# Kernel tuning notes

Measured on AMD Instinct MI355X. Metric: run time of the kernel, lower is better.

Reference implementation:

```python
import math
import jax, jax.numpy as jnp
import numpy as np

B, T = 64, 8192
D_OUT = 128
KPOS = 2
DT = 1.0 / 240.0


def _ema(x, alpha):
    # x: [B, T] -> causal EMA along T: acc = alpha*acc + (1-alpha)*x_t, acc0 = 0
    def step(acc, xt):
        acc = alpha * acc + (1.0 - alpha) * xt
        return acc, acc
    _, ys = jax.lax.scan(step, jnp.zeros(x.shape[0], x.dtype), x.T)  # ys: [T, B]
    return ys.T


def _fourier_axis(coord, logw, phi):
    # coord: [B,T]; logw, phi: [K] -> [B,T,2K]
    w = jnp.exp(logw)[None, None, :]
    arg = 2.0 * math.pi * coord[..., None] * w + phi[None, None, :]
    return jnp.concatenate([jnp.sin(arg), jnp.cos(arg)], axis=-1)


def setup_inputs() -> dict:
    key = jax.random.key(0)
    ks = jax.random.split(key, 4)
    gaze_xy = jax.random.normal(ks[0], (B, T, 2), dtype=jnp.float32) * 5.0
    D_in = 4 * KPOS + 12  # 20
    # xavier-uniform style init for the two Linear layers
    lim1 = math.sqrt(6.0 / (D_in + D_OUT))
    lim2 = math.sqrt(6.0 / (D_OUT + D_OUT))
    W1 = jax.random.uniform(ks[1], (D_in, D_OUT), jnp.float32, -lim1, lim1)
    b1 = jnp.zeros((D_OUT,), jnp.float32)
    W2 = jax.random.uniform(ks[2], (D_OUT, D_OUT), jnp.float32, -lim2, lim2)
    b2 = jnp.zeros((D_OUT,), jnp.float32)
    return {
        "gaze_xy": gaze_xy,
        "pos_logw_x": jnp.full((KPOS,), math.log(1.0 / 64.0), jnp.float32),
        "pos_phi_x": jnp.zeros((KPOS,), jnp.float32),
        "pos_logw_y": jnp.full((KPOS,), math.log(1.0 / 64.0), jnp.float32),
        "pos_phi_y": jnp.zeros((KPOS,), jnp.float32),
        "sac_log_thr": jnp.asarray(math.log(200.0), jnp.float32),
        "sac_invT": jnp.asarray(0.05, jnp.float32),
        "W1": W1, "b1": b1, "W2": W2, "b2": b2,
    }


def reference(gaze_xy, pos_logw_x, pos_phi_x, pos_logw_y, pos_phi_y,
              sac_log_thr, sac_invT, W1, b1, W2, b2):
    dt = max(DT, 1e-6)
    eps = 1e-6
    # causal diff with first-frame prepend (diff at t=0 is zero)
    prev = jnp.concatenate([gaze_xy[:, :1], gaze_xy[:, :-1]], axis=1)
    v = (gaze_xy - prev) / dt                      # [B,T,2]
    v_prev = jnp.concatenate([v[:, :1], v[:, :-1]], axis=1)
    a = (v - v_prev) / dt                          # [B,T,2]
    speed = jnp.linalg.norm(v, axis=-1)            # [B,T]
    inv_sp = 1.0 / (speed + eps)
    dir_cos = v[..., 0] * inv_sp
    dir_sin = v[..., 1] * inv_sp
    a_par = (v * a).sum(-1) * inv_sp
    a_perp = (v[..., 0] * a[..., 1] - v[..., 1] * a[..., 0]) * inv_sp
    thr = jnp.exp(sac_log_thr)
    gate = jax.nn.sigmoid(sac_invT * (speed - thr))  # [B,T]
    q_fast = _ema(gate, 0.8)
    q_slow = _ema(gate, 0.95)
    scalars = jnp.stack([v[..., 0], v[..., 1], speed, dir_cos, dir_sin,
                         a[..., 0], a[..., 1], a_par, a_perp,
                         gate, q_fast, q_slow], axis=-1)  # [B,T,12]
    fx = _fourier_axis(gaze_xy[..., 0], pos_logw_x, pos_phi_x)  # [B,T,4]
    fy = _fourier_axis(gaze_xy[..., 1], pos_logw_y, pos_phi_y)  # [B,T,4]
    feats = jnp.concatenate([fx, fy, scalars], axis=-1)         # [B,T,20]
    h = jax.nn.gelu(feats @ W1 + b1, approximate=False)
    h = jax.nn.gelu(h @ W2 + b2, approximate=False)
    return h
```

## Files before the change

### kernel.cpp

```cpp
#include <hip/hip_runtime.h>
#include <math.h>

#define BB 64
#define TT 8192
#define NTILES 8192
#define MLP_GRID 768
#define EMA_GRID 512

typedef short short8 __attribute__((ext_vector_type(8)));
typedef float f32x4 __attribute__((ext_vector_type(4)));

__device__ __forceinline__ unsigned short f2bf(float x) {
    unsigned int u = __float_as_uint(x);
    u += 0x7fffu + ((u >> 16) & 1u);
    return (unsigned short)(u >> 16);
}

__device__ __forceinline__ unsigned int f2bf2(float lo, float hi) {
    return (unsigned int)f2bf(lo) | ((unsigned int)f2bf(hi) << 16);
}

__device__ __forceinline__ float fast_sigmoid(float z) {
    return __builtin_amdgcn_rcpf(1.0f + __expf(-z));
}

__device__ __forceinline__ float fast_gelu(float x) {
    return x * fast_sigmoid(1.702f * x);
}

__global__ __launch_bounds__(256) void ema_kernel(
    const float* __restrict__ gaze, const float* __restrict__ logthr,
    const float* __restrict__ invT, float* __restrict__ qf, float* __restrict__ qs)
{
    __shared__ __align__(16) float sg[1280];
    const int tid = threadIdx.x;
    const int b   = blockIdx.x >> 3;
    const int t0  = (blockIdx.x & 7) << 10;
    const float thr = __expf(logthr[0]);
    const float sT  = invT[0];
    const float2* gz = (const float2*)gaze + (size_t)b * TT;

    #pragma unroll
    for (int it = 0; it < 5; ++it) {
        int i = tid + it * 256;
        int t = t0 - 252 + i;
        float val = 0.0f;
        if (t >= 0 && t < TT) {
            float vx = 0.0f, vy = 0.0f;
            if (t > 0) {
                float2 a = gz[t], p = gz[t - 1];
                vx = (a.x - p.x) * 240.0f;
                vy = (a.y - p.y) * 240.0f;
            }
            float speed = sqrtf(vx * vx + vy * vy);
            val = 1.0f / (1.0f + __expf(-sT * (speed - thr)));
        }
        sg[i] = val;
    }
    __syncthreads();

    const float4* sg4 = (const float4*)sg;
    float Sf = 0.0f, Ss = 0.0f;
    float wf = 0.16f;
    float ws = 0.0475f;
    for (int u = 62; u >= 0; --u) {
        float4 qv = sg4[tid + u];
        float hf = fmaf(0.8f,  fmaf(0.8f,  fmaf(0.8f,  qv.x, qv.y), qv.z), qv.w);
        Sf = fmaf(wf, hf, Sf);  wf *= 0.4096f;
        float hs = fmaf(0.95f, fmaf(0.95f, fmaf(0.95f, qv.x, qv.y), qv.z), qv.w);
        Ss = fmaf(ws, hs, Ss);  ws *= 0.81450625f;
    }
    float4 r = sg4[tid + 63];
    float g0v = r.x, g1v = r.y, g2v = r.z, g3v = r.w;

    float o0 = Sf + 0.2f * g0v;
    float o1 = fmaf(0.8f,   Sf, 0.2f * fmaf(0.8f, g0v, g1v));
    float o2 = fmaf(0.64f,  Sf, 0.2f * (g2v + 0.8f * g1v + 0.64f * g0v));
    float o3 = fmaf(0.512f, Sf, 0.2f * (g3v + 0.8f * g2v + 0.64f * g1v + 0.512f * g0v));

    float p0 = Ss + 0.05f * g0v;
    float p1 = fmaf(0.95f,     Ss, 0.05f * fmaf(0.95f, g0v, g1v));
    float p2 = fmaf(0.9025f,   Ss, 0.05f * (g2v + 0.95f * g1v + 0.9025f * g0v));
    float p3 = fmaf(0.857375f, Ss, 0.05f * (g3v + 0.95f * g2v + 0.9025f * g1v + 0.857375f * g0v));

    const size_t ob = (size_t)b * TT + t0 + 4 * tid;
    *(float4*)(qf + ob) = make_float4(o0, o1, o2, o3);
    *(float4*)(qs + ob) = make_float4(p0, p1, p2, p3);
}

__global__ __launch_bounds__(256, 3) void mlp_kernel(
    const float* __restrict__ gaze,
    const float* __restrict__ lwx, const float* __restrict__ phx,
    const float* __restrict__ lwy, const float* __restrict__ phy,
    const float* __restrict__ logthr, const float* __restrict__ invT,
    const float* __restrict__ W1, const float* __restrict__ b1,
    const float* __restrict__ W2, const float* __restrict__ b2,
    const float* __restrict__ qf, const float* __restrict__ qs,
    float* __restrict__ out)
{
    __shared__ __align__(16) unsigned short sW2[128 * 136];
    __shared__ __align__(16) unsigned short sh1[4][16 * 136];

    const int tid  = threadIdx.x;
    const int wave = tid >> 6;
    const int lane = tid & 63;
    const int c    = lane & 15;
    const int q    = lane >> 4;

    #pragma unroll
    for (int it = 0; it < 32; ++it) {
        int i  = tid + it * 256;
        int n  = i & 127;
        int kp = i >> 7;
        unsigned short lo = f2bf(W2[(2 * kp) * 128 + n]);
        unsigned short hi = f2bf(W2[(2 * kp + 1) * 128 + n]);
        *(unsigned int*)&sW2[n * 136 + 2 * kp] = ((unsigned int)hi << 16) | lo;
    }

    short8 B1[8];
    #pragma unroll
    for (int j = 0; j < 8; ++j) {
        union { unsigned short u[8]; short8 v; } tmp;
        #pragma unroll
        for (int u = 0; u < 8; ++u) {
            int k = 8 * q + u;
            float w = 0.0f;
            if (k < 20)       w = W1[k * 128 + 16 * j + c];
            else if (k == 20) w = b1[16 * j + c];
            tmp.u[u] = (k <= 20) ? f2bf(w) : (unsigned short)0;
        }
        B1[j] = tmp.v;
    }

    f32x4 bias2v[8];
    #pragma unroll
    for (int j = 0; j < 8; ++j)
        bias2v[j] = *(const f32x4*)&b2[16 * j + 4 * q];

    const float twopi = 6.283185307179586f;
    const float cwx0 = twopi * __expf(lwx[0]), cwx1 = twopi * __expf(lwx[1]);
    const float cwy0 = twopi * __expf(lwy[0]), cwy1 = twopi * __expf(lwy[1]);
    const float px0 = phx[0], px1 = phx[1], py0 = phy[0], py1 = phy[1];
    const float thr = __expf(logthr[0]), sT = invT[0];

    __syncthreads();

    unsigned short* h1w = sh1[wave];
    const float2* gz = (const float2*)gaze;

    for (int tile = blockIdx.x; tile < NTILES; tile += MLP_GRID) {
        const int b   = tile >> 7;
        const int t0  = (tile & 127) << 6;
        const int t   = t0 + wave * 16 + c;
        const int idx = b * TT + t;

        float2 g0 = gz[idx];
        float2 g1 = (t > 0) ? gz[idx - 1] : g0;
        float2 g2 = (t > 1) ? gz[idx - 2] : g1;
        float vx = (g0.x - g1.x) * 240.0f;
        float vy = (g0.y - g1.y) * 240.0f;
        float vpx = (g1.x - g2.x) * 240.0f;
        float vpy = (g1.y - g2.y) * 240.0f;
        float ax = (vx - vpx) * 240.0f;
        float ay = (vy - vpy) * 240.0f;
        float speed  = sqrtf(vx * vx + vy * vy);
        float inv_sp = __builtin_amdgcn_rcpf(speed + 1e-6f);

        float f[8] = {0.f, 0.f, 0.f, 0.f, 0.f, 0.f, 0.f, 0.f};
        if (q == 0) {
            __sincosf(fmaf(g0.x, cwx0, px0), &f[0], &f[2]);
            __sincosf(fmaf(g0.x, cwx1, px1), &f[1], &f[3]);
            __sincosf(fmaf(g0.y, cwy0, py0), &f[4], &f[6]);
            __sincosf(fmaf(g0.y, cwy1, py1), &f[5], &f[7]);
        } else if (q == 1) {
            f[0] = vx; f[1] = vy; f[2] = speed;
            f[3] = vx * inv_sp; f[4] = vy * inv_sp;
            f[5] = ax; f[6] = ay;
            f[7] = (vx * ax + vy * ay) * inv_sp;
        } else if (q == 2) {
            f[0] = (vx * ay - vy * ax) * inv_sp;
            f[1] = fast_sigmoid(sT * (speed - thr));
            f[2] = qf[idx];
            f[3] = qs[idx];
            f[4] = 1.0f;
        }

        union { unsigned short u[8]; short8 v; } A1;
        #pragma unroll
        for (int k = 0; k < 8; ++k) A1.u[k] = f2bf(f[k]);

        #pragma unroll
        for (int j = 0; j < 8; ++j) {
            f32x4 acc = {0.f, 0.f, 0.f, 0.f};
            acc = __builtin_amdgcn_mfma_f32_16x16x32_bf16(B1[j], A1.v, acc, 0, 0, 0);
            unsigned int lo = f2bf2(fast_gelu(acc[0]), fast_gelu(acc[1]));
            unsigned int hi = f2bf2(fast_gelu(acc[2]), fast_gelu(acc[3]));
            *(uint2*)&h1w[c * 136 + 16 * j + 4 * q] = make_uint2(lo, hi);
        }
        asm volatile("s_waitcnt lgkmcnt(0)" ::: "memory");

        short8 A2[4];
        #pragma unroll
        for (int s = 0; s < 4; ++s)
            A2[s] = *(const short8*)&h1w[c * 136 + 32 * s + 8 * q];

        float* ob = out + (size_t)(b * TT + t0 + wave * 16 + c) * 128 + 4 * q;
        #pragma unroll
        for (int j = 0; j < 8; ++j) {
            f32x4 acc = bias2v[j];
            #pragma unroll
            for (int s = 0; s < 4; ++s) {
                short8 W2f = *(const short8*)&sW2[(16 * j + c) * 136 + 32 * s + 8 * q];
                acc = __builtin_amdgcn_mfma_f32_16x16x32_bf16(W2f, A2[s], acc, 0, 0, 0);
            }
            f32x4 o;
            #pragma unroll
            for (int r = 0; r < 4; ++r) o[r] = fast_gelu(acc[r]);
            __builtin_nontemporal_store(o, (f32x4*)(ob + 16 * j));
        }
    }
}

extern "C" void kernel_launch(void* const* d_in, const int* in_sizes, int n_in,
                              void* d_out, int out_size, void* d_ws, size_t ws_size,
                              hipStream_t stream)
{
    const float* gaze   = (const float*)d_in[0];
    const float* lwx    = (const float*)d_in[1];
    const float* phx    = (const float*)d_in[2];
    const float* lwy    = (const float*)d_in[3];
    const float* phy    = (const float*)d_in[4];
    const float* logthr = (const float*)d_in[5];
    const float* invT   = (const float*)d_in[6];
    const float* W1     = (const float*)d_in[7];
    const float* b1     = (const float*)d_in[8];
    const float* W2     = (const float*)d_in[9];
    const float* b2     = (const float*)d_in[10];
    float* out = (float*)d_out;

    float* qf = (float*)d_ws;
    float* qs = qf + BB * TT;

    ema_kernel<<<EMA_GRID, 256, 0, stream>>>(gaze, logthr, invT, qf, qs);
    mlp_kernel<<<MLP_GRID, 256, 0, stream>>>(gaze, lwx, phx, lwy, phy, logthr, invT,
                                             W1, b1, W2, b2, qf, qs, out);
}
```

Before: 327.2 us.

## Use 512-thread MLP blocks with software-prefetched inputs and LDS bias

The MLP kernel now runs 8 waves per block, each covering 128 time steps per tile, on a grid of 512 blocks. The gaze and EMA inputs for the next tile are loaded into registers while the current tile is computed, so global load latency is hidden. The b2 bias moves from registers to shared memory to cut register pressure for the higher occupancy target. This costs extra registers for the prefetched values and a per-tile LDS read of the bias.

New measurement: 339.1 us. +3.6%, slower.

```diff
diff --git a/kernel.cpp b/kernel.cpp
--- a/kernel.cpp
+++ b/kernel.cpp
@@ -3,8 +3,8 @@
 
 #define BB 64
 #define TT 8192
-#define NTILES 8192
-#define MLP_GRID 768
+#define NT2 4096
+#define MLP_GRID 512
 #define EMA_GRID 512
 
 typedef short short8 __attribute__((ext_vector_type(8)));
@@ -88,7 +88,7 @@
     *(float4*)(qs + ob) = make_float4(p0, p1, p2, p3);
 }
 
-__global__ __launch_bounds__(256, 3) void mlp_kernel(
+__global__ __launch_bounds__(512, 4) void mlp_kernel(
     const float* __restrict__ gaze,
     const float* __restrict__ lwx, const float* __restrict__ phx,
     const float* __restrict__ lwy, const float* __restrict__ phy,
@@ -99,7 +99,8 @@
     float* __restrict__ out)
 {
     __shared__ __align__(16) unsigned short sW2[128 * 136];
-    __shared__ __align__(16) unsigned short sh1[4][16 * 136];
+    __shared__ __align__(16) unsigned short sh1[8][16 * 136];
+    __shared__ __align__(16) float sb2[128];
 
     const int tid  = threadIdx.x;
     const int wave = tid >> 6;
@@ -108,14 +109,15 @@
     const int q    = lane >> 4;
 
     #pragma unroll
-    for (int it = 0; it < 32; ++it) {
-        int i  = tid + it * 256;
+    for (int it = 0; it < 16; ++it) {
+        int i  = tid + it * 512;
         int n  = i & 127;
         int kp = i >> 7;
         unsigned short lo = f2bf(W2[(2 * kp) * 128 + n]);
         unsigned short hi = f2bf(W2[(2 * kp + 1) * 128 + n]);
         *(unsigned int*)&sW2[n * 136 + 2 * kp] = ((unsigned int)hi << 16) | lo;
     }
+    if (tid < 128) sb2[tid] = b2[tid];
 
     short8 B1[8];
     #pragma unroll
@@ -132,11 +134,6 @@
         B1[j] = tmp.v;
     }
 
-    f32x4 bias2v[8];
-    #pragma unroll
-    for (int j = 0; j < 8; ++j)
-        bias2v[j] = *(const f32x4*)&b2[16 * j + 4 * q];
-
     const float twopi = 6.283185307179586f;
     const float cwx0 = twopi * __expf(lwx[0]), cwx1 = twopi * __expf(lwx[1]);
     const float cwy0 = twopi * __expf(lwy[0]), cwy1 = twopi * __expf(lwy[1]);
@@ -148,15 +145,35 @@
     unsigned short* h1w = sh1[wave];
     const float2* gz = (const float2*)gaze;
 
-    for (int tile = blockIdx.x; tile < NTILES; tile += MLP_GRID) {
-        const int b   = tile >> 7;
-        const int t0  = (tile & 127) << 6;
+    int tile = blockIdx.x;
+    float2 g0, g1, g2; float qfv = 0.f, qsv = 0.f;
+    {
+        const int b   = tile >> 6;
+        const int t   = ((tile & 63) << 7) + wave * 16 + c;
+        const int idx = b * TT + t;
+        g0 = gz[idx];
+        g1 = (t > 0) ? gz[idx - 1] : g0;
+        g2 = (t > 1) ? gz[idx - 2] : g1;
+        if (q == 2) { qfv = qf[idx]; qsv = qs[idx]; }
+    }
+
+    for (; tile < NT2; tile += MLP_GRID) {
+        const int b   = tile >> 6;
+        const int t0  = (tile & 63) << 7;
         const int t   = t0 + wave * 16 + c;
-        const int idx = b * TT + t;
-
-        float2 g0 = gz[idx];
-        float2 g1 = (t > 0) ? gz[idx - 1] : g0;
-        float2 g2 = (t > 1) ? gz[idx - 2] : g1;
+
+        float2 n0 = g0, n1 = g1, n2 = g2; float nqf = 0.f, nqs = 0.f;
+        const int ntile = tile + MLP_GRID;
+        if (ntile < NT2) {
+            const int nb   = ntile >> 6;
+            const int nt   = ((ntile & 63) << 7) + wave * 16 + c;
+            const int nidx = nb * TT + nt;
+            n0 = gz[nidx];
+            n1 = (nt > 0) ? gz[nidx - 1] : n0;
+            n2 = (nt > 1) ? gz[nidx - 2] : n1;
+            if (q == 2) { nqf = qf[nidx]; nqs = qs[nidx]; }
+        }
+
         float vx = (g0.x - g1.x) * 240.0f;
         float vy = (g0.y - g1.y) * 240.0f;
         float vpx = (g1.x - g2.x) * 240.0f;
@@ -180,8 +197,8 @@
         } else if (q == 2) {
             f[0] = (vx * ay - vy * ax) * inv_sp;
             f[1] = fast_sigmoid(sT * (speed - thr));
-            f[2] = qf[idx];
-            f[3] = qs[idx];
+            f[2] = qfv;
+            f[3] = qsv;
             f[4] = 1.0f;
         }
 
@@ -207,7 +224,7 @@
         float* ob = out + (size_t)(b * TT + t0 + wave * 16 + c) * 128 + 4 * q;
         #pragma unroll
         for (int j = 0; j < 8; ++j) {
-            f32x4 acc = bias2v[j];
+            f32x4 acc = *(const f32x4*)&sb2[16 * j + 4 * q];
             #pragma unroll
             for (int s = 0; s < 4; ++s) {
                 short8 W2f = *(const short8*)&sW2[(16 * j + c) * 136 + 32 * s + 8 * q];
@@ -218,6 +235,8 @@
             for (int r = 0; r < 4; ++r) o[r] = fast_gelu(acc[r]);
             __builtin_nontemporal_store(o, (f32x4*)(ob + 16 * j));
         }
+
+        g0 = n0; g1 = n1; g2 = n2; qfv = nqf; qsv = nqs;
     }
 }
 
@@ -242,6 +261,6 @@
     float* qs = qf + BB * TT;
 
     ema_kernel<<<EMA_GRID, 256, 0, stream>>>(gaze, logthr, invT, qf, qs);
-    mlp_kernel<<<MLP_GRID, 256, 0, stream>>>(gaze, lwx, phx, lwy, phy, logthr, invT,
+    mlp_kernel<<<MLP_GRID, 512, 0, stream>>>(gaze, lwx, phx, lwy, phy, logthr, invT,
                                              W1, b1, W2, b2, qf, qs, out);
 }
```

## Pre-convert weights to bf16 in prep kernel and read them from global/L1

Applied to the files above, without the earlier changes.

Adds a small prep kernel that converts W1 (plus bias row) and W2 to bf16 in the workspace once per call. The MLP kernel drops its per-block LDS staging of W2 and its register-held W1 fragments, and instead loads weight fragments from global memory inside the tile loop, relying on cache. It also raises occupancy (launch bounds 4, grid 1024). This removes per-block conversion work and frees LDS and registers, at the cost of repeated global/L1 weight loads per tile and an extra kernel launch.

New measurement: 398.5 us. 1.22x slower.

```diff
diff --git a/kernel.cpp b/kernel.cpp
--- a/kernel.cpp
+++ b/kernel.cpp
@@ -4,7 +4,7 @@
 #define BB 64
 #define TT 8192
 #define NTILES 8192
-#define MLP_GRID 768
+#define MLP_GRID 1024
 #define EMA_GRID 512
 
 typedef short short8 __attribute__((ext_vector_type(8)));
@@ -26,6 +26,25 @@
 
 __device__ __forceinline__ float fast_gelu(float x) {
     return x * fast_sigmoid(1.702f * x);
+}
+
+__global__ __launch_bounds__(256) void prep_kernel(
+    const float* __restrict__ W1, const float* __restrict__ b1,
+    const float* __restrict__ W2,
+    unsigned short* __restrict__ w1bf, unsigned short* __restrict__ w2bf)
+{
+    const int tid = threadIdx.x;
+    const int bid = blockIdx.x;
+    if (bid < 64) {
+        int i  = bid * 256 + tid;
+        int ch = i >> 7, k = i & 127;
+        w2bf[i] = f2bf(W2[k * 128 + ch]);
+    } else {
+        int i  = (bid - 64) * 256 + tid;
+        int ch = i >> 5, k = i & 31;
+        float v = (k < 20) ? W1[k * 128 + ch] : ((k == 20) ? b1[ch] : 0.0f);
+        w1bf[i] = f2bf(v);
+    }
 }
 
 __global__ __launch_bounds__(256) void ema_kernel(
@@ -88,17 +107,16 @@
     *(float4*)(qs + ob) = make_float4(p0, p1, p2, p3);
 }
 
-__global__ __launch_bounds__(256, 3) void mlp_kernel(
+__global__ __launch_bounds__(256, 4) void mlp_kernel(
     const float* __restrict__ gaze,
     const float* __restrict__ lwx, const float* __restrict__ phx,
     const float* __restrict__ lwy, const float* __restrict__ phy,
     const float* __restrict__ logthr, const float* __restrict__ invT,
-    const float* __restrict__ W1, const float* __restrict__ b1,
-    const float* __restrict__ W2, const float* __restrict__ b2,
+    const unsigned short* __restrict__ w1bf, const unsigned short* __restrict__ w2bf,
+    const float* __restrict__ b2,
     const float* __restrict__ qf, const float* __restrict__ qs,
     float* __restrict__ out)
 {
-    __shared__ __align__(16) unsigned short sW2[128 * 136];
     __shared__ __align__(16) unsigned short sh1[4][16 * 136];
 
     const int tid  = threadIdx.x;
@@ -107,44 +125,12 @@
     const int c    = lane & 15;
     const int q    = lane >> 4;
 
-    #pragma unroll
-    for (int it = 0; it < 32; ++it) {
-        int i  = tid + it * 256;
-        int n  = i & 127;
-        int kp = i >> 7;
-        unsigned short lo = f2bf(W2[(2 * kp) * 128 + n]);
-        unsigned short hi = f2bf(W2[(2 * kp + 1) * 128 + n]);
-        *(unsigned int*)&sW2[n * 136 + 2 * kp] = ((unsigned int)hi << 16) | lo;
-    }
-
-    short8 B1[8];
-    #pragma unroll
-    for (int j = 0; j < 8; ++j) {
-        union { unsigned short u[8]; short8 v; } tmp;
-        #pragma unroll
-        for (int u = 0; u < 8; ++u) {
-            int k = 8 * q + u;
-            float w = 0.0f;
-            if (k < 20)       w = W1[k * 128 + 16 * j + c];
-            else if (k == 20) w = b1[16 * j + c];
-            tmp.u[u] = (k <= 20) ? f2bf(w) : (unsigned short)0;
-        }
-        B1[j] = tmp.v;
-    }
-
-    f32x4 bias2v[8];
-    #pragma unroll
-    for (int j = 0; j < 8; ++j)
-        bias2v[j] = *(const f32x4*)&b2[16 * j + 4 * q];
-
     const float twopi = 6.283185307179586f;
     const float cwx0 = twopi * __expf(lwx[0]), cwx1 = twopi * __expf(lwx[1]);
     const float cwy0 = twopi * __expf(lwy[0]), cwy1 = twopi * __expf(lwy[1]);
     const float px0 = phx[0], px1 = phx[1], py0 = phy[0], py1 = phy[1];
     const float thr = __expf(logthr[0]), sT = invT[0];
 
-    __syncthreads();
-
     unsigned short* h1w = sh1[wave];
     const float2* gz = (const float2*)gaze;
 
@@ -153,6 +139,14 @@
         const int t0  = (tile & 127) << 6;
         const int t   = t0 + wave * 16 + c;
         const int idx = b * TT + t;
+
+        unsigned long long a1 = (unsigned long long)w1bf;
+        unsigned long long a2 = (unsigned long long)w2bf;
+        unsigned long long a3 = (unsigned long long)b2;
+        asm volatile("" : "+s"(a1), "+s"(a2), "+s"(a3));
+        const unsigned short* w1p = (const unsigned short*)a1;
+        const unsigned short* w2p = (const unsigned short*)a2;
+        const float*          b2p = (const float*)a3;
 
         float2 g0 = gz[idx];
         float2 g1 = (t > 0) ? gz[idx - 1] : g0;
@@ -191,8 +185,9 @@
 
         #pragma unroll
         for (int j = 0; j < 8; ++j) {
+            short8 B1j = *(const short8*)&w1p[(16 * j + c) * 32 + 8 * q];
             f32x4 acc = {0.f, 0.f, 0.f, 0.f};
-            acc = __builtin_amdgcn_mfma_f32_16x16x32_bf16(B1[j], A1.v, acc, 0, 0, 0);
+            acc = __builtin_amdgcn_mfma_f32_16x16x32_bf16(B1j, A1.v, acc, 0, 0, 0);
             unsigned int lo = f2bf2(fast_gelu(acc[0]), fast_gelu(acc[1]));
             unsigned int hi = f2bf2(fast_gelu(acc[2]), fast_gelu(acc[3]));
             *(uint2*)&h1w[c * 136 + 16 * j + 4 * q] = make_uint2(lo, hi);
@@ -207,10 +202,10 @@
         float* ob = out + (size_t)(b * TT + t0 + wave * 16 + c) * 128 + 4 * q;
         #pragma unroll
         for (int j = 0; j < 8; ++j) {
-            f32x4 acc = bias2v[j];
+            f32x4 acc = *(const f32x4*)&b2p[16 * j + 4 * q];
             #pragma unroll
             for (int s = 0; s < 4; ++s) {
-                short8 W2f = *(const short8*)&sW2[(16 * j + c) * 136 + 32 * s + 8 * q];
+                short8 W2f = *(const short8*)&w2p[(16 * j + c) * 128 + 32 * s + 8 * q];
                 acc = __builtin_amdgcn_mfma_f32_16x16x32_bf16(W2f, A2[s], acc, 0, 0, 0);
             }
             f32x4 o;
@@ -240,8 +235,11 @@
 
     float* qf = (float*)d_ws;
     float* qs = qf + BB * TT;
-
+    unsigned short* w1bf = (unsigned short*)(qs + BB * TT);
+    unsigned short* w2bf = w1bf + 128 * 32;
+
+    prep_kernel<<<80, 256, 0, stream>>>(W1, b1, W2, w1bf, w2bf);
     ema_kernel<<<EMA_GRID, 256, 0, stream>>>(gaze, logthr, invT, qf, qs);
     mlp_kernel<<<MLP_GRID, 256, 0, stream>>>(gaze, lwx, phx, lwy, phy, logthr, invT,
-                                             W1, b1, W2, b2, qf, qs, out);
-}
+                                             w1bf, w2bf, b2, qf, qs, out);
+}
```

## Permute W1 columns so layer-1 MFMA output feeds layer-2 directly in registers

Applied to the files above, without the earlier changes.

Reorders the hidden-channel mapping of W1/b1 so each lane's layer-1 accumulator values line up with the bf16 A-operand layout needed by the layer-2 MFMA. This removes the per-wave shared-memory round trip and its wait for the hidden activations. The b2 bias moves from registers to LDS, and the grid grows with launch bounds raised to 4 blocks per SIMD to increase occupancy, which tightens the register budget and could cause spills.

Result: no change. 326.6 us (-0.2%).

```diff
diff --git a/kernel.cpp b/kernel.cpp
--- a/kernel.cpp
+++ b/kernel.cpp
@@ -4,7 +4,7 @@
 #define BB 64
 #define TT 8192
 #define NTILES 8192
-#define MLP_GRID 768
+#define MLP_GRID 2048
 #define EMA_GRID 512
 
 typedef short short8 __attribute__((ext_vector_type(8)));
@@ -88,7 +88,7 @@
     *(float4*)(qs + ob) = make_float4(p0, p1, p2, p3);
 }
 
-__global__ __launch_bounds__(256, 3) void mlp_kernel(
+__global__ __launch_bounds__(256, 4) void mlp_kernel(
     const float* __restrict__ gaze,
     const float* __restrict__ lwx, const float* __restrict__ phx,
     const float* __restrict__ lwy, const float* __restrict__ phy,
@@ -99,11 +99,11 @@
     float* __restrict__ out)
 {
     __shared__ __align__(16) unsigned short sW2[128 * 136];
-    __shared__ __align__(16) unsigned short sh1[4][16 * 136];
+    __shared__ __align__(16) float sb2[128];
 
     const int tid  = threadIdx.x;
+    const int lane = tid & 63;
     const int wave = tid >> 6;
-    const int lane = tid & 63;
     const int c    = lane & 15;
     const int q    = lane >> 4;
 
@@ -116,26 +116,23 @@
         unsigned short hi = f2bf(W2[(2 * kp + 1) * 128 + n]);
         *(unsigned int*)&sW2[n * 136 + 2 * kp] = ((unsigned int)hi << 16) | lo;
     }
+    if (tid < 128) sb2[tid] = b2[tid];
 
     short8 B1[8];
     #pragma unroll
     for (int j = 0; j < 8; ++j) {
+        const int ch = 32 * (j & 3) + 8 * (c >> 2) + 4 * (j >> 2) + (c & 3);
         union { unsigned short u[8]; short8 v; } tmp;
         #pragma unroll
         for (int u = 0; u < 8; ++u) {
             int k = 8 * q + u;
             float w = 0.0f;
-            if (k < 20)       w = W1[k * 128 + 16 * j + c];
-            else if (k == 20) w = b1[16 * j + c];
+            if (k < 20)       w = W1[k * 128 + ch];
+            else if (k == 20) w = b1[ch];
             tmp.u[u] = (k <= 20) ? f2bf(w) : (unsigned short)0;
         }
         B1[j] = tmp.v;
     }
-
-    f32x4 bias2v[8];
-    #pragma unroll
-    for (int j = 0; j < 8; ++j)
-        bias2v[j] = *(const f32x4*)&b2[16 * j + 4 * q];
 
     const float twopi = 6.283185307179586f;
     const float cwx0 = twopi * __expf(lwx[0]), cwx1 = twopi * __expf(lwx[1]);
@@ -145,7 +142,6 @@
 
     __syncthreads();
 
-    unsigned short* h1w = sh1[wave];
     const float2* gz = (const float2*)gaze;
 
     for (int tile = blockIdx.x; tile < NTILES; tile += MLP_GRID) {
@@ -189,25 +185,28 @@
         #pragma unroll
         for (int k = 0; k < 8; ++k) A1.u[k] = f2bf(f[k]);
 
+        f32x4 acc1[8];
         #pragma unroll
         for (int j = 0; j < 8; ++j) {
-            f32x4 acc = {0.f, 0.f, 0.f, 0.f};
-            acc = __builtin_amdgcn_mfma_f32_16x16x32_bf16(B1[j], A1.v, acc, 0, 0, 0);
-            unsigned int lo = f2bf2(fast_gelu(acc[0]), fast_gelu(acc[1]));
-            unsigned int hi = f2bf2(fast_gelu(acc[2]), fast_gelu(acc[3]));
-            *(uint2*)&h1w[c * 136 + 16 * j + 4 * q] = make_uint2(lo, hi);
-        }
-        asm volatile("s_waitcnt lgkmcnt(0)" ::: "memory");
+            f32x4 z = {0.f, 0.f, 0.f, 0.f};
+            acc1[j] = __builtin_amdgcn_mfma_f32_16x16x32_bf16(B1[j], A1.v, z, 0, 0, 0);
+        }
 
         short8 A2[4];
         #pragma unroll
-        for (int s = 0; s < 4; ++s)
-            A2[s] = *(const short8*)&h1w[c * 136 + 32 * s + 8 * q];
+        for (int s = 0; s < 4; ++s) {
+            union { unsigned int w[4]; short8 v; } t2;
+            t2.w[0] = f2bf2(fast_gelu(acc1[s][0]),     fast_gelu(acc1[s][1]));
+            t2.w[1] = f2bf2(fast_gelu(acc1[s][2]),     fast_gelu(acc1[s][3]));
+            t2.w[2] = f2bf2(fast_gelu(acc1[s + 4][0]), fast_gelu(acc1[s + 4][1]));
+            t2.w[3] = f2bf2(fast_gelu(acc1[s + 4][2]), fast_gelu(acc1[s + 4][3]));
+            A2[s] = t2.v;
+        }
 
         float* ob = out + (size_t)(b * TT + t0 + wave * 16 + c) * 128 + 4 * q;
         #pragma unroll
         for (int j = 0; j < 8; ++j) {
-            f32x4 acc = bias2v[j];
+            f32x4 acc = *(const f32x4*)&sb2[16 * j + 4 * q];
             #pragma unroll
             for (int s = 0; s < 4; ++s) {
                 short8 W2f = *(const short8*)&sW2[(16 * j + c) * 136 + 32 * s + 8 * q];
```
